# Optimization experiments

Hardware: AMD Instinct MI355X
Metric: run time of the kernel (lower is better)

The kernel has to match this reference:

```python
import jax, jax.numpy as jnp
import numpy as np

B, C, H, W = 8, 64, 64, 64
CK = C // 8  # query/key channels

def setup_inputs() -> dict:
    key = jax.random.key(0)
    ks = jax.random.split(key, 8)
    x = jax.random.normal(ks[0], (B, C, H, W), dtype=jnp.float32)
    # Conv1d with kernel size 1 == per-position linear map; store weights as [out, in].
    # (Spectral norm only rescales the weight matrix; with given weights the forward
    #  math is an ordinary 1x1 conv.)
    Wq = jax.random.normal(ks[1], (CK, C), dtype=jnp.float32) / np.sqrt(C)
    bq = jnp.zeros((CK,), dtype=jnp.float32)
    Wk = jax.random.normal(ks[2], (CK, C), dtype=jnp.float32) / np.sqrt(C)
    bk = jnp.zeros((CK,), dtype=jnp.float32)
    Wv = jax.random.normal(ks[3], (C, C), dtype=jnp.float32) / np.sqrt(C)
    bv = jnp.zeros((C,), dtype=jnp.float32)
    gamma = jnp.asarray(0.5, dtype=jnp.float32)  # nonzero so attention path matters
    return {"x": x, "Wq": Wq, "bq": bq, "Wk": Wk, "bk": bk, "Wv": Wv, "bv": bv, "gamma": gamma}

def reference(x, Wq, bq, Wk, bk, Wv, bv, gamma):
    b, c, h, w = x.shape
    flat = x.reshape(b, c, h * w)                       # [B, C, L]
    q = jnp.einsum('oc,bcl->blo', Wq, flat) + bq        # [B, L, C/8] (query permuted)
    k = jnp.einsum('oc,bcl->bol', Wk, flat) + bk[None, :, None]   # [B, C/8, L]
    v = jnp.einsum('oc,bcl->bol', Wv, flat) + bv[None, :, None]   # [B, C, L]
    qk = jnp.einsum('blo,bom->blm', q, k)               # [B, L, L]
    attn = jax.nn.softmax(qk, axis=1)                   # softmax over dim 1 (rows)
    out = jnp.einsum('bcl,blm->bcm', v, attn)           # [B, C, L]
    out = out.reshape(b, c, h, w)
    return gamma * out + x
```

## Files before the change

kernel.cpp:

```cpp
#include <hip/hip_runtime.h>
#include <math.h>

#define B_   8
#define C_   64
#define CK_  8
#define L_   4096

typedef __attribute__((ext_vector_type(8))) __bf16 bf16x8;
typedef __attribute__((ext_vector_type(4))) __bf16 bf16x4;
typedef __attribute__((ext_vector_type(4))) float  f32x4;
typedef __attribute__((ext_vector_type(4))) short  s16x4;

__global__ __launch_bounds__(256) void qkv_kernel(
    const float* __restrict__ x,
    const float* __restrict__ Wq, const float* __restrict__ bq,
    const float* __restrict__ Wk, const float* __restrict__ bk,
    const float* __restrict__ Wv, const float* __restrict__ bv,
    __bf16* __restrict__ qo, __bf16* __restrict__ ko, __bf16* __restrict__ vpack)
{
    __shared__ float LWq[CK_ * C_];
    __shared__ float LWk[CK_ * C_];
    __shared__ float LWv[C_ * C_];
    __shared__ __bf16 Lqs[64 * 8];
    __shared__ __bf16 Lks[64 * 8];

    const int tid = threadIdx.x;
    if (tid < 128) {
        ((float4*)LWq)[tid] = ((const float4*)Wq)[tid];
        ((float4*)LWk)[tid] = ((const float4*)Wk)[tid];
    }
    #pragma unroll
    for (int j = 0; j < 4; ++j)
        ((float4*)LWv)[tid + j * 256] = ((const float4*)Wv)[tid + j * 256];
    __syncthreads();

    const int b  = blockIdx.x >> 6;
    const int t  = blockIdx.x & 63;
    const int l0 = t << 6;
    const int lg = tid & 15;
    const int g  = tid >> 4;

    float va[4][4];
    float qk[4];
    #pragma unroll
    for (int j = 0; j < 4; ++j) {
        float bb = bv[4 * g + j];
        va[j][0] = bb; va[j][1] = bb; va[j][2] = bb; va[j][3] = bb;
    }
    {
        float bb = (g < 8) ? bq[g] : bk[g - 8];
        qk[0] = bb; qk[1] = bb; qk[2] = bb; qk[3] = bb;
    }
    const float* wqk = (g < 8) ? (LWq + g * C_) : (LWk + (g - 8) * C_);

    const float* xp = x + ((size_t)b * C_) * L_ + l0 + lg * 4;
    #pragma unroll 4
    for (int c4 = 0; c4 < 16; ++c4) {
        float4 xv[4];
        #pragma unroll
        for (int u = 0; u < 4; ++u)
            xv[u] = *(const float4*)(xp + (size_t)(4 * c4 + u) * L_);
        #pragma unroll
        for (int j = 0; j < 4; ++j) {
            float4 wv = ((const float4*)(LWv + (4 * g + j) * C_))[c4];
            float* a = va[j];
            a[0]=fmaf(wv.x,xv[0].x,a[0]); a[1]=fmaf(wv.x,xv[0].y,a[1]); a[2]=fmaf(wv.x,xv[0].z,a[2]); a[3]=fmaf(wv.x,xv[0].w,a[3]);
            a[0]=fmaf(wv.y,xv[1].x,a[0]); a[1]=fmaf(wv.y,xv[1].y,a[1]); a[2]=fmaf(wv.y,xv[1].z,a[2]); a[3]=fmaf(wv.y,xv[1].w,a[3]);
            a[0]=fmaf(wv.z,xv[2].x,a[0]); a[1]=fmaf(wv.z,xv[2].y,a[1]); a[2]=fmaf(wv.z,xv[2].z,a[2]); a[3]=fmaf(wv.z,xv[2].w,a[3]);
            a[0]=fmaf(wv.w,xv[3].x,a[0]); a[1]=fmaf(wv.w,xv[3].y,a[1]); a[2]=fmaf(wv.w,xv[3].z,a[2]); a[3]=fmaf(wv.w,xv[3].w,a[3]);
        }
        {
            float4 wv = ((const float4*)wqk)[c4];
            qk[0]=fmaf(wv.x,xv[0].x,qk[0]); qk[1]=fmaf(wv.x,xv[0].y,qk[1]); qk[2]=fmaf(wv.x,xv[0].z,qk[2]); qk[3]=fmaf(wv.x,xv[0].w,qk[3]);
            qk[0]=fmaf(wv.y,xv[1].x,qk[0]); qk[1]=fmaf(wv.y,xv[1].y,qk[1]); qk[2]=fmaf(wv.y,xv[1].z,qk[2]); qk[3]=fmaf(wv.y,xv[1].w,qk[3]);
            qk[0]=fmaf(wv.z,xv[2].x,qk[0]); qk[1]=fmaf(wv.z,xv[2].y,qk[1]); qk[2]=fmaf(wv.z,xv[2].z,qk[2]); qk[3]=fmaf(wv.z,xv[2].w,qk[3]);
            qk[0]=fmaf(wv.w,xv[3].x,qk[0]); qk[1]=fmaf(wv.w,xv[3].y,qk[1]); qk[2]=fmaf(wv.w,xv[3].z,qk[2]); qk[3]=fmaf(wv.w,xv[3].w,qk[3]);
        }
    }

    {
        __bf16* vt = vpack + ((size_t)b * 64 + t) * 4096;
        const int cb = g >> 2;
        const int sg = lg >> 2;
        const int qd = lg & 3;
        #pragma unroll
        for (int j = 0; j < 4; ++j) {
            bf16x4 vv;
            vv[0]=(__bf16)va[j][0]; vv[1]=(__bf16)va[j][1]; vv[2]=(__bf16)va[j][2]; vv[3]=(__bf16)va[j][3];
            *(bf16x4*)(vt + ((size_t)((cb * 4 + sg) * 64 + qd * 16 + (g & 3) * 4 + j)) * 4) = vv;
        }
    }
    #pragma unroll
    for (int u = 0; u < 4; ++u) {
        if (g < 8) Lqs[(lg * 4 + u) * 8 + g]       = (__bf16)qk[u];
        else       Lks[(lg * 4 + u) * 8 + (g - 8)] = (__bf16)qk[u];
    }
    __syncthreads();
    if (tid < 64) {
        *(bf16x8*)(qo + ((size_t)b * L_ + l0 + tid) * 8) = *(bf16x8*)(Lqs + tid * 8);
        *(bf16x8*)(ko + ((size_t)b * L_ + l0 + tid) * 8) = *(bf16x8*)(Lks + tid * 8);
    }
}

__global__ __launch_bounds__(512, 4) void attn_kernel(
    const __bf16* __restrict__ q, const __bf16* __restrict__ kT,
    const __bf16* __restrict__ VP, const float* __restrict__ x,
    const float* __restrict__ gamma_p, float* __restrict__ out)
{
    __shared__ __bf16 Lv[2][2][4096];
    __shared__ float  Sc[4096];
    __shared__ float  csA[8][16];

    const int tid  = threadIdx.x;
    const int w    = tid >> 6;
    const int lane = tid & 63;
    const int quad = lane >> 4;
    const int l16  = lane & 15;
    const int wh   = w & 3;
    const int lh   = w >> 2;
    const int mb   = blockIdx.x & 63;
    const int b    = blockIdx.x >> 6;
    const int m0   = mb << 6;

    const __bf16* vp = VP + (size_t)b * (64 * 4096);
    const __bf16* qb = q  + (size_t)b * L_ * CK_;

    bf16x8 kf = {};
    if (quad == 0) kf = *(const bf16x8*)(kT + ((size_t)b * L_ + m0 + wh * 16 + l16) * CK_);

    const int tA = (w * 2) >> 3,     sA = (w * 2) & 7;
    const int tB = (w * 2 + 1) >> 3, sB = (w * 2 + 1) & 7;
    const __bf16* gA = vp + (size_t)(tA * 32) * 4096 + sA * 512 + lane * 8;
    const __bf16* gB = vp + (size_t)(tB * 32) * 4096 + sB * 512 + lane * 8;
    const int dA = sA * 512 + lane * 8;
    const int dB = sB * 512 + lane * 8;

    f32x4 acc[4] = {};
    float csum = 0.f;
    bf16x8 qc[4], qn[4];
    bf16x8 rA, rB;

    rA = *(const bf16x8*)gA;
    rB = *(const bf16x8*)gB;
    *(bf16x8*)(&Lv[0][tA][dA]) = rA;
    *(bf16x8*)(&Lv[0][tB][dB]) = rB;
    #pragma unroll
    for (int sg = 0; sg < 4; ++sg) {
        bf16x8 tq = {};
        if (quad == 0) tq = *(const bf16x8*)(qb + (size_t)((lh * 32) * 64 + sg * 16 + l16) * CK_);
        qc[sg] = tq;
    }

    for (int s = 0; s < 32; ++s) {
        __syncthreads();

        if (s + 1 < 32) {
            rA = *(const bf16x8*)(gA + (size_t)(s + 1) * 4096);
            rB = *(const bf16x8*)(gB + (size_t)(s + 1) * 4096);
            #pragma unroll
            for (int sg = 0; sg < 4; ++sg) {
                bf16x8 tq = {};
                if (quad == 0) tq = *(const bf16x8*)(qb + (size_t)((lh * 32 + s + 1) * 64 + sg * 16 + l16) * CK_);
                qn[sg] = tq;
            }
        }

        const __bf16* Lb = &Lv[s & 1][lh][0];
        #pragma unroll
        for (int sg = 0; sg < 4; ++sg) {
            f32x4 sv = __builtin_amdgcn_mfma_f32_16x16x32_bf16(qc[sg], kf, (f32x4){0.f,0.f,0.f,0.f}, 0, 0, 0);
            const float e0 = __expf(sv[0]);
            const float e1 = __expf(sv[1]);
            const float e2 = __expf(sv[2]);
            const float e3 = __expf(sv[3]);
            csum += (e0 + e1) + (e2 + e3);
            bf16x4 pk;
            pk[0] = (__bf16)e0; pk[1] = (__bf16)e1; pk[2] = (__bf16)e2; pk[3] = (__bf16)e3;
            s16x4 pb = __builtin_bit_cast(s16x4, pk);
            #pragma unroll
            for (int cb = 0; cb < 4; ++cb) {
                s16x4 vf = *(const s16x4*)(Lb + ((size_t)((cb * 4 + sg) * 64 + lane)) * 4);
                acc[cb] = __builtin_amdgcn_mfma_f32_16x16x16bf16_1k(vf, pb, acc[cb], 0, 0, 0);
            }
        }

        if (s + 1 < 32) {
            const int nb = (s + 1) & 1;
            *(bf16x8*)(&Lv[nb][tA][dA]) = rA;
            *(bf16x8*)(&Lv[nb][tB][dB]) = rB;
        }
        #pragma unroll
        for (int sg = 0; sg < 4; ++sg) qc[sg] = qn[sg];
    }

    if (lh == 1) {
        #pragma unroll
        for (int cb = 0; cb < 4; ++cb)
            #pragma unroll
            for (int r = 0; r < 4; ++r)
                Sc[(wh * 64 + cb * 16 + quad * 4 + r) * 16 + l16] = acc[cb][r];
    }
    csum += __shfl_xor(csum, 16);
    csum += __shfl_xor(csum, 32);
    if (quad == 0) csA[w][l16] = csum;
    __syncthreads();

    if (lh == 0) {
        const float rinv = gamma_p[0] / (csA[wh][l16] + csA[wh + 4][l16]);
        #pragma unroll
        for (int cb = 0; cb < 4; ++cb) {
            #pragma unroll
            for (int r = 0; r < 4; ++r) {
                const int c = cb * 16 + quad * 4 + r;
                const float vsum = acc[cb][r] + Sc[(wh * 64 + c) * 16 + l16];
                const size_t idx = ((size_t)(b * 64 + c)) * L_ + m0 + wh * 16 + l16;
                out[idx] = fmaf(rinv, vsum, x[idx]);
            }
        }
    }
}

extern "C" void kernel_launch(void* const* d_in, const int* in_sizes, int n_in,
                              void* d_out, int out_size, void* d_ws, size_t ws_size,
                              hipStream_t stream) {
    const float* x  = (const float*)d_in[0];
    const float* Wq = (const float*)d_in[1];
    const float* bq = (const float*)d_in[2];
    const float* Wk = (const float*)d_in[3];
    const float* bk = (const float*)d_in[4];
    const float* Wv = (const float*)d_in[5];
    const float* bv = (const float*)d_in[6];
    const float* gm = (const float*)d_in[7];
    float* out = (float*)d_out;

    __bf16* ws    = (__bf16*)d_ws;
    __bf16* qo    = ws;
    __bf16* ko    = ws + 262144;
    __bf16* vpack = ws + 524288;

    qkv_kernel<<<dim3(B_ * (L_ / 64)), dim3(256), 0, stream>>>(
        x, Wq, bq, Wk, bk, Wv, bv, qo, ko, vpack);
    attn_kernel<<<dim3(B_ * 64), dim3(512), 0, stream>>>(
        qo, ko, vpack, x, gm, out);
}
```

Before: 132.7 us.

## Process two key tiles per iteration using wider bf16 MFMA for PV

The attention loop now handles two 64-wide L slices per iteration, 16 iterations instead of 32. The two slices' probabilities and V fragments are concatenated so the PV product uses the 16x16x32 bf16 MFMA rather than 16x16x16, halving the PV MFMA count and the number of barriers. The V staging buffer doubles to four tiles per stage and the cross-wave reduction scratch now reuses it. The q prefetch across iterations is dropped in favour of in-loop loads, and the larger LDS footprint may reduce how many blocks fit per CU.

```diff
diff --git a/kernel.cpp b/kernel.cpp
--- a/kernel.cpp
+++ b/kernel.cpp
@@ -9,7 +9,6 @@
 typedef __attribute__((ext_vector_type(8))) __bf16 bf16x8;
 typedef __attribute__((ext_vector_type(4))) __bf16 bf16x4;
 typedef __attribute__((ext_vector_type(4))) float  f32x4;
-typedef __attribute__((ext_vector_type(4))) short  s16x4;
 
 __global__ __launch_bounds__(256) void qkv_kernel(
     const float* __restrict__ x,
@@ -107,8 +106,7 @@
     const __bf16* __restrict__ VP, const float* __restrict__ x,
     const float* __restrict__ gamma_p, float* __restrict__ out)
 {
-    __shared__ __bf16 Lv[2][2][4096];
-    __shared__ float  Sc[4096];
+    __shared__ __bf16 Lv[2][4][4096];
     __shared__ float  csA[8][16];
 
     const int tid  = threadIdx.x;
@@ -128,77 +126,91 @@
     bf16x8 kf = {};
     if (quad == 0) kf = *(const bf16x8*)(kT + ((size_t)b * L_ + m0 + wh * 16 + l16) * CK_);
 
-    const int tA = (w * 2) >> 3,     sA = (w * 2) & 7;
-    const int tB = (w * 2 + 1) >> 3, sB = (w * 2 + 1) & 7;
-    const __bf16* gA = vp + (size_t)(tA * 32) * 4096 + sA * 512 + lane * 8;
-    const __bf16* gB = vp + (size_t)(tB * 32) * 4096 + sB * 512 + lane * 8;
-    const int dA = sA * 512 + lane * 8;
-    const int dB = sB * 512 + lane * 8;
+    const __bf16* gk[4];
+    int ok[4];
+    #pragma unroll
+    for (int k = 0; k < 4; ++k) {
+        const int u = w * 4 + k, tl = u >> 3, seg = u & 7;
+        gk[k] = vp + (size_t)((tl & 1) * 32 + (tl >> 1)) * 4096 + seg * 512 + lane * 8;
+        ok[k] = tl * 4096 + seg * 512 + lane * 8;
+    }
 
     f32x4 acc[4] = {};
     float csum = 0.f;
-    bf16x8 qc[4], qn[4];
-    bf16x8 rA, rB;
-
-    rA = *(const bf16x8*)gA;
-    rB = *(const bf16x8*)gB;
-    *(bf16x8*)(&Lv[0][tA][dA]) = rA;
-    *(bf16x8*)(&Lv[0][tB][dB]) = rB;
-    #pragma unroll
-    for (int sg = 0; sg < 4; ++sg) {
-        bf16x8 tq = {};
-        if (quad == 0) tq = *(const bf16x8*)(qb + (size_t)((lh * 32) * 64 + sg * 16 + l16) * CK_);
-        qc[sg] = tq;
-    }
-
-    for (int s = 0; s < 32; ++s) {
+    bf16x8 r[4];
+
+    #pragma unroll
+    for (int k = 0; k < 4; ++k) r[k] = *(const bf16x8*)gk[k];
+    #pragma unroll
+    for (int k = 0; k < 4; ++k) *(bf16x8*)(&Lv[0][0][0] + ok[k]) = r[k];
+
+    for (int i = 0; i < 16; ++i) {
         __syncthreads();
 
-        if (s + 1 < 32) {
-            rA = *(const bf16x8*)(gA + (size_t)(s + 1) * 4096);
-            rB = *(const bf16x8*)(gB + (size_t)(s + 1) * 4096);
-            #pragma unroll
-            for (int sg = 0; sg < 4; ++sg) {
-                bf16x8 tq = {};
-                if (quad == 0) tq = *(const bf16x8*)(qb + (size_t)((lh * 32 + s + 1) * 64 + sg * 16 + l16) * CK_);
-                qn[sg] = tq;
-            }
-        }
-
-        const __bf16* Lb = &Lv[s & 1][lh][0];
-        #pragma unroll
-        for (int sg = 0; sg < 4; ++sg) {
-            f32x4 sv = __builtin_amdgcn_mfma_f32_16x16x32_bf16(qc[sg], kf, (f32x4){0.f,0.f,0.f,0.f}, 0, 0, 0);
+        if (i < 15) {
+            #pragma unroll
+            for (int k = 0; k < 4; ++k)
+                r[k] = *(const bf16x8*)(gk[k] + (size_t)(i + 1) * 8192);
+        }
+
+        bf16x8 qA[4], qB[4];
+        #pragma unroll
+        for (int sg = 0; sg < 4; ++sg) {
+            qA[sg] = *(const bf16x8*)(qb + (size_t)((lh * 32 + 2 * i)     * 64 + sg * 16 + l16) * CK_);
+            qB[sg] = *(const bf16x8*)(qb + (size_t)((lh * 32 + 2 * i + 1) * 64 + sg * 16 + l16) * CK_);
+        }
+
+        bf16x4 pkA[4], pkB[4];
+        #pragma unroll
+        for (int sg = 0; sg < 4; ++sg) {
+            f32x4 sv = __builtin_amdgcn_mfma_f32_16x16x32_bf16(qA[sg], kf, (f32x4){0.f,0.f,0.f,0.f}, 0, 0, 0);
             const float e0 = __expf(sv[0]);
             const float e1 = __expf(sv[1]);
             const float e2 = __expf(sv[2]);
             const float e3 = __expf(sv[3]);
             csum += (e0 + e1) + (e2 + e3);
-            bf16x4 pk;
-            pk[0] = (__bf16)e0; pk[1] = (__bf16)e1; pk[2] = (__bf16)e2; pk[3] = (__bf16)e3;
-            s16x4 pb = __builtin_bit_cast(s16x4, pk);
+            pkA[sg][0]=(__bf16)e0; pkA[sg][1]=(__bf16)e1; pkA[sg][2]=(__bf16)e2; pkA[sg][3]=(__bf16)e3;
+        }
+        #pragma unroll
+        for (int sg = 0; sg < 4; ++sg) {
+            f32x4 sv = __builtin_amdgcn_mfma_f32_16x16x32_bf16(qB[sg], kf, (f32x4){0.f,0.f,0.f,0.f}, 0, 0, 0);
+            const float e0 = __expf(sv[0]);
+            const float e1 = __expf(sv[1]);
+            const float e2 = __expf(sv[2]);
+            const float e3 = __expf(sv[3]);
+            csum += (e0 + e1) + (e2 + e3);
+            pkB[sg][0]=(__bf16)e0; pkB[sg][1]=(__bf16)e1; pkB[sg][2]=(__bf16)e2; pkB[sg][3]=(__bf16)e3;
+        }
+
+        const __bf16* LbA = &Lv[i & 1][lh][0];
+        const __bf16* LbB = &Lv[i & 1][2 + lh][0];
+        #pragma unroll
+        for (int sg = 0; sg < 4; ++sg) {
+            bf16x8 p8 = __builtin_shufflevector(pkA[sg], pkB[sg], 0, 1, 2, 3, 4, 5, 6, 7);
             #pragma unroll
             for (int cb = 0; cb < 4; ++cb) {
-                s16x4 vf = *(const s16x4*)(Lb + ((size_t)((cb * 4 + sg) * 64 + lane)) * 4);
-                acc[cb] = __builtin_amdgcn_mfma_f32_16x16x16bf16_1k(vf, pb, acc[cb], 0, 0, 0);
+                bf16x4 vfA = *(const bf16x4*)(LbA + ((size_t)((cb * 4 + sg) * 64 + lane)) * 4);
+                bf16x4 vfB = *(const bf16x4*)(LbB + ((size_t)((cb * 4 + sg) * 64 + lane)) * 4);
+                bf16x8 a8 = __builtin_shufflevector(vfA, vfB, 0, 1, 2, 3, 4, 5, 6, 7);
+                acc[cb] = __builtin_amdgcn_mfma_f32_16x16x32_bf16(a8, p8, acc[cb], 0, 0, 0);
             }
         }
 
-        if (s + 1 < 32) {
-            const int nb = (s + 1) & 1;
-            *(bf16x8*)(&Lv[nb][tA][dA]) = rA;
-            *(bf16x8*)(&Lv[nb][tB][dB]) = rB;
-        }
-        #pragma unroll
-        for (int sg = 0; sg < 4; ++sg) qc[sg] = qn[sg];
-    }
-
+        if (i < 15) {
+            const int nb = (i + 1) & 1;
+            #pragma unroll
+            for (int k = 0; k < 4; ++k)
+                *(bf16x8*)(&Lv[nb][0][0] + ok[k]) = r[k];
+        }
+    }
+
+    float* Sc = (float*)&Lv[0][0][0];
     if (lh == 1) {
         #pragma unroll
         for (int cb = 0; cb < 4; ++cb)
             #pragma unroll
-            for (int r = 0; r < 4; ++r)
-                Sc[(wh * 64 + cb * 16 + quad * 4 + r) * 16 + l16] = acc[cb][r];
+            for (int r2 = 0; r2 < 4; ++r2)
+                Sc[(wh * 64 + cb * 16 + quad * 4 + r2) * 16 + l16] = acc[cb][r2];
     }
     csum += __shfl_xor(csum, 16);
     csum += __shfl_xor(csum, 32);
@@ -210,9 +222,9 @@
         #pragma unroll
         for (int cb = 0; cb < 4; ++cb) {
             #pragma unroll
-            for (int r = 0; r < 4; ++r) {
-                const int c = cb * 16 + quad * 4 + r;
-                const float vsum = acc[cb][r] + Sc[(wh * 64 + c) * 16 + l16];
+            for (int r2 = 0; r2 < 4; ++r2) {
+                const int c = cb * 16 + quad * 4 + r2;
+                const float vsum = acc[cb][r2] + Sc[(wh * 64 + c) * 16 + l16];
                 const size_t idx = ((size_t)(b * 64 + c)) * L_ + m0 + wh * 16 + l16;
                 out[idx] = fmaf(rinv, vsum, x[idx]);
             }
```

After: 126.8 us. 4.4% less time.
